# Kernel optimization log

Hardware: AMD Instinct MI355X
Metric: run time of the kernel (lower is better)

## Reference

```python
import jax, jax.numpy as jnp
import numpy as np

ANGLE_BITS = 3          # TurboQuantConfig.angle_bits default
LEVELS = 2 ** ANGLE_BITS
PI = np.pi


def _angle_ranges(d_minus_1, dtype):
    # hyperspherical coords: first d-2 angles in [0, pi], last angle in [0, 2*pi)
    return jnp.concatenate([
        jnp.full((d_minus_1 - 1,), PI, dtype),
        jnp.full((1,), 2.0 * PI, dtype),
    ])


def polar_compress(x):
    """x: [..., d] -> (r [...,1], theta_indices int32 [..., d-1])."""
    # suffix norms s_i = ||x[i:]|| via reversed cumsum of squares
    suffix = jnp.sqrt(jnp.cumsum((x * x)[..., ::-1], axis=-1)[..., ::-1])
    r = suffix[..., :1]
    cos_t = jnp.clip(x[..., :-1] / jnp.maximum(suffix[..., :-1], 1e-12), -1.0, 1.0)
    theta = jnp.arccos(cos_t)                      # [..., d-1], in [0, pi]
    # last angle carries the sign of x[..., -1]: map to [0, 2*pi)
    last = jnp.where(x[..., -1:] < 0, 2.0 * PI - theta[..., -1:], theta[..., -1:])
    theta = jnp.concatenate([theta[..., :-1], last], axis=-1)
    ranges = _angle_ranges(theta.shape[-1], theta.dtype)
    idx = jnp.round(theta / ranges * (LEVELS - 1)).astype(jnp.int32)
    return r, idx


def polar_decompress(r, idx):
    """(r [...,1], idx [..., d-1]) -> x_hat [..., d] via trig products."""
    d1 = idx.shape[-1]
    ranges = _angle_ranges(d1, r.dtype)
    theta = idx.astype(r.dtype) / (LEVELS - 1) * ranges
    sinp = jnp.cumprod(jnp.sin(theta), axis=-1)                 # [..., d-1]
    prods = jnp.concatenate([jnp.ones_like(r), sinp], axis=-1)  # [..., d]
    coss = jnp.concatenate([jnp.cos(theta), jnp.ones_like(r)], axis=-1)
    return r * prods * coss


def setup_inputs() -> dict:
    key = jax.random.key(0)
    kq, kk, kv, kn = jax.random.split(key, 4)
    B, H, T, k, d = 1, 32, 8192, 16, 128
    return {
        "queries": jax.random.normal(kq, (B, H, k, d), jnp.float32),
        "keys": jax.random.normal(kk, (B, H, T, d), jnp.float32),
        "values": jax.random.normal(kv, (B, H, T, d), jnp.float32),
        # faithful stand-in for `torch.randn_like(scores) * 0.01` QJL correction,
        # materialized deterministically as an input
        "qjl_noise": jax.random.normal(kn, (B, H, k, T), jnp.float32) * 0.01,
    }


def reference(queries, keys, values, qjl_noise):
    d = queries.shape[-1]
    # compress_kv_cache: polar angle quantization of keys and values
    r_k, idx_k = polar_compress(keys)
    r_v, idx_v = polar_compress(values)
    # compute_attention_with_compressed_kv: decompress-then-attend
    keys_polar = polar_decompress(r_k, idx_k)      # [B,H,T,d]
    values_polar = polar_decompress(r_v, idx_v)    # [B,H,T,d]
    scores = jnp.einsum('bhkd,bhtd->bhkt', queries, keys_polar) / jnp.sqrt(
        jnp.asarray(d, queries.dtype))
    scores = scores + qjl_noise
    attn = jax.nn.softmax(scores, axis=-1)
    return jnp.einsum('bhkt,bhtd->bhkd', attn, values_polar)
```

## Files before the change

kernel.cpp:

```cpp
#include <hip/hip_runtime.h>
#include <math.h>

typedef __attribute__((ext_vector_type(8))) short bf16x8;
typedef __attribute__((ext_vector_type(4))) float f32x4;
typedef __attribute__((ext_vector_type(2))) float f32x2;

#define HEADS 32
#define SEQT  8192
#define DIM   128
#define NQ    16
#define BPH   64
#define BTOK  128
#define WTOK  32
#define TILE  16
#define NPART BPH
#define PSTR  132
#define QPAD  136
#define QSCALE 0.08838834764831845f

#define OFF_QS    0
#define OFF_PS    4352
#define OFF_LUT   8448
#define OFF_ML    8576
#define OFF_KS    9088
#define OFF_MERGE 9088
#define LDS_BYTES 26496

#define DPP_ROW_SHL(N) (0x100 | (N))
#define DPP_ROW_SHR(N) (0x110 | (N))
#define DPP_QP_XOR1   0xB1
#define DPP_QP_XOR2   0x4E
#define DPP_HALF_MIRR 0x141
#define DPP_MIRR      0x140

template <int CTRL>
__device__ __forceinline__ float dpp0(float v) {
  return __int_as_float(__builtin_amdgcn_update_dpp(
      0, __float_as_int(v), CTRL, 0xF, 0xF, true));
}
template <int CTRL>
__device__ __forceinline__ float dpp1(float v) {
  return __int_as_float(__builtin_amdgcn_update_dpp(
      __float_as_int(1.0f), __float_as_int(v), CTRL, 0xF, 0xF, false));
}
__device__ __forceinline__ float rmax16(float v) {
  v = fmaxf(v, dpp0<DPP_QP_XOR1>(v));
  v = fmaxf(v, dpp0<DPP_QP_XOR2>(v));
  v = fmaxf(v, dpp0<DPP_HALF_MIRR>(v));
  v = fmaxf(v, dpp0<DPP_MIRR>(v));
  return v;
}
__device__ __forceinline__ float rsum16(float v) {
  v += dpp0<DPP_QP_XOR1>(v);
  v += dpp0<DPP_QP_XOR2>(v);
  v += dpp0<DPP_HALF_MIRR>(v);
  v += dpp0<DPP_MIRR>(v);
  return v;
}
__device__ __forceinline__ float rdlane(float v, int l) {
  return __int_as_float(__builtin_amdgcn_readlane(__float_as_int(v), l));
}
__device__ __forceinline__ unsigned short f2bf(float f) {
  unsigned u = __float_as_uint(f);
  u += 0x7FFFu + ((u >> 16) & 1u);
  return (unsigned short)(u >> 16);
}
__device__ __forceinline__ int idx7c(float c) {
  int i = 0;
  i += c <  0.9749279121818236f;
  i += c <  0.7818314824680298f;
  i += c <  0.4338837391175581f;
  i += c <  6.123233995736766e-17f;
  i += c < -0.4338837391175581f;
  i += c < -0.7818314824680298f;
  i += c < -0.9749279121818236f;
  return i;
}

__device__ __forceinline__ float2 polar_rt(float x0, float x1, int lane,
                                           const float2* lutA, const float2* lutB) {
  float a = x0 * x0;
  float p = fmaf(x1, x1, a);
  float v = p;
  v += dpp0<DPP_ROW_SHL(1)>(v);
  v += dpp0<DPP_ROW_SHL(2)>(v);
  v += dpp0<DPP_ROW_SHL(4)>(v);
  v += dpp0<DPP_ROW_SHL(8)>(v);
  float R0 = rdlane(v, 0), R1 = rdlane(v, 16), R2 = rdlane(v, 32), R3 = rdlane(v, 48);
  float T2 = R3, T1 = R2 + R3, T0 = R1 + T1;
  int row = lane >> 4;
  float T = (row == 0) ? T0 : ((row == 1) ? T1 : ((row == 2) ? T2 : 0.f));
  float ss0 = v + T;
  float total = R0 + T0;
  float ss1 = ss0 - a;
  float c0 = x0 * __builtin_amdgcn_rsqf(ss0);
  float c1 = x1 * __builtin_amdgcn_rsqf(ss1);
  float rad = sqrtf(total);
  float2 sc0 = lutA[idx7c(c0)];
  float2 sc1 = lutA[idx7c(c1)];
  if (lane == 63) {
    int ib = 0;
    ib += c0 <  0.9009688679024191f;
    ib += c0 <  0.2225209339563144f;
    ib += c0 < -0.6234898018587336f;
    int i0 = (x1 < 0.f) ? (7 - ib) : ib;
    sc0 = lutB[i0];
    sc1 = make_float2(1.f, 1.f);
  }
  float qp = sc0.x * sc1.x;
  float w = qp;
  w *= dpp1<DPP_ROW_SHR(1)>(w);
  w *= dpp1<DPP_ROW_SHR(2)>(w);
  w *= dpp1<DPP_ROW_SHR(4)>(w);
  w *= dpp1<DPP_ROW_SHR(8)>(w);
  float e = dpp1<DPP_ROW_SHR(1)>(w);
  float F0 = rdlane(w, 15), F1 = rdlane(w, 31), F2 = rdlane(w, 47);
  float M1 = F0, M2 = F0 * F1, M3 = M2 * F2;
  float M = (row == 0) ? 1.f : ((row == 1) ? M1 : ((row == 2) ? M2 : M3));
  float E = e * M;
  float rE = rad * E;
  return make_float2(rE * sc0.y, rE * sc0.x * sc1.y);
}

__global__ __launch_bounds__(256, 4)
void attn_partial(const float* __restrict__ Q, const float* __restrict__ K,
                  const float* __restrict__ V, const float* __restrict__ noise,
                  float* __restrict__ part) {
  __shared__ __align__(16) char RAW[LDS_BYTES];
  unsigned short* Qs  = (unsigned short*)(RAW + OFF_QS);
  float*          Ps  = (float*)(RAW + OFF_PS);
  float2*         lutA = (float2*)(RAW + OFF_LUT);
  float2*         lutB = lutA + 8;
  float2*         Ml  = (float2*)(RAW + OFF_ML);
  unsigned short* Ks  = (unsigned short*)(RAW + OFF_KS);

  const int tid  = threadIdx.x;
  const int lane = tid & 63;
  const int wv   = tid >> 6;
  const int h    = blockIdx.x / BPH;
  const int bh   = blockIdx.x % BPH;

  if (tid < 8) {
    float fi = (float)tid / 7.0f;
    float ta = fi * 3.14159274101257324f;
    float tb = fi * 6.28318548202514648f;
    lutA[tid] = make_float2(sinf(ta), cosf(ta));
    lutB[tid] = make_float2(sinf(tb), cosf(tb));
  }
  {
    const float* Qh = Q + (size_t)h * NQ * DIM;
    for (int i = tid; i < NQ * DIM; i += 256)
      Qs[(i >> 7) * QPAD + (i & 127)] = f2bf(Qh[i] * QSCALE);
  }
  __syncthreads();

  const int G = lane >> 4, r16 = lane & 15;
  bf16x8 qa[4];
#pragma unroll
  for (int c = 0; c < 4; ++c)
    qa[c] = *(const bf16x8*)&Qs[r16 * QPAD + c * 32 + G * 8];

  f32x2 acc[NQ];
#pragma unroll
  for (int qq = 0; qq < NQ; ++qq) acc[qq] = (f32x2){0.f, 0.f};
  float m_r[4] = {-INFINITY, -INFINITY, -INFINITY, -INFINITY};
  float l_r[4] = {0.f, 0.f, 0.f, 0.f};

  const size_t hoff = (size_t)h * SEQT * DIM;
  const int t0 = bh * BTOK + wv * WTOK;
  const float2* Kp = (const float2*)(K + hoff + (size_t)t0 * DIM) + lane;
  const float2* Vp = (const float2*)(V + hoff + (size_t)t0 * DIM) + lane;
  const float* nh = noise + (size_t)h * NQ * SEQT + t0 + r16;
  unsigned short* myK = Ks + wv * TILE * QPAD;
  float* myP = Ps + wv * TILE * NQ;

#pragma unroll 1
  for (int tile = 0; tile < WTOK / TILE; ++tile) {
#pragma unroll 4
    for (int tt = 0; tt < TILE; ++tt) {
      float2 xv = Kp[(tile * TILE + tt) * 64];
      float2 kh = polar_rt(xv.x, xv.y, lane, lutA, lutB);
      unsigned pk = (unsigned)f2bf(kh.x) | ((unsigned)f2bf(kh.y) << 16);
      ((unsigned*)&myK[tt * QPAD])[lane] = pk;
    }
    f32x4 d0 = {0.f, 0.f, 0.f, 0.f};
#pragma unroll
    for (int c = 0; c < 4; ++c) {
      bf16x8 b0 = *(const bf16x8*)&myK[r16 * QPAD + c * 32 + G * 8];
      d0 = __builtin_amdgcn_mfma_f32_16x16x32_bf16(qa[c], b0, d0, 0, 0, 0);
    }
    const float* nt = nh + tile * TILE;
    float s0_[4];
#pragma unroll
    for (int rr = 0; rr < 4; ++rr)
      s0_[rr] = d0[rr] + nt[(size_t)(4 * G + rr) * SEQT];
    float al_r[4];
#pragma unroll
    for (int rr = 0; rr < 4; ++rr) {
      float mt = rmax16(s0_[rr]);
      float mn = fmaxf(m_r[rr], mt);
      al_r[rr] = __expf(m_r[rr] - mn);
      m_r[rr] = mn;
    }
    float p0[4];
#pragma unroll
    for (int rr = 0; rr < 4; ++rr) {
      p0[rr] = __expf(s0_[rr] - m_r[rr]);
      l_r[rr] = l_r[rr] * al_r[rr] + rsum16(p0[rr]);
    }
    *(float4*)&myP[r16 * NQ + 4 * G] = make_float4(p0[0], p0[1], p0[2], p0[3]);
#pragma unroll
    for (int qq = 0; qq < NQ; ++qq) {
      float alq = rdlane(al_r[qq & 3], (qq >> 2) << 4);
      acc[qq] *= (f32x2){alq, alq};
    }
#pragma unroll 2
    for (int tt = 0; tt < TILE; ++tt) {
      float2 xv = Vp[(tile * TILE + tt) * 64];
      float2 vh = polar_rt(xv.x, xv.y, lane, lutA, lutB);
      f32x2 vh2 = {vh.x, vh.y};
      const float* pv = &myP[tt * NQ];
      float4 pa = ((const float4*)pv)[0];
      float4 pb = ((const float4*)pv)[1];
      float4 pc = ((const float4*)pv)[2];
      float4 pd = ((const float4*)pv)[3];
      float pq[NQ] = {pa.x, pa.y, pa.z, pa.w, pb.x, pb.y, pb.z, pb.w,
                      pc.x, pc.y, pc.z, pc.w, pd.x, pd.y, pd.z, pd.w};
#pragma unroll
      for (int qq = 0; qq < NQ; ++qq)
        acc[qq] = __builtin_elementwise_fma((f32x2){pq[qq], pq[qq]}, vh2, acc[qq]);
    }
  }

  if (r16 == 0) {
#pragma unroll
    for (int rr = 0; rr < 4; ++rr)
      Ml[wv * NQ + 4 * G + rr] = make_float2(m_r[rr], l_r[rr]);
  }
  __syncthreads();
#pragma unroll
  for (int qq = 0; qq < NQ; ++qq) {
    float2 e0 = Ml[0 * NQ + qq], e1 = Ml[1 * NQ + qq];
    float2 e2 = Ml[2 * NQ + qq], e3 = Ml[3 * NQ + qq];
    float Mq = fmaxf(fmaxf(e0.x, e1.x), fmaxf(e2.x, e3.x));
    float own = (wv == 0) ? e0.x : ((wv == 1) ? e1.x : ((wv == 2) ? e2.x : e3.x));
    float al = __expf(own - Mq);
    acc[qq] *= (f32x2){al, al};
  }
  float* buf = (float*)(RAW + OFF_MERGE);
  if (wv >= 2) {
#pragma unroll
    for (int qq = 0; qq < NQ; ++qq)
      *(float2*)&buf[(wv - 2) * 2048 + qq * 128 + 2 * lane] =
          make_float2(acc[qq].x, acc[qq].y);
  }
  __syncthreads();
  if (wv < 2) {
#pragma unroll
    for (int qq = 0; qq < NQ; ++qq) {
      float2 t = *(const float2*)&buf[wv * 2048 + qq * 128 + 2 * lane];
      acc[qq] += (f32x2){t.x, t.y};
    }
  }
  __syncthreads();
  if (wv == 1) {
#pragma unroll
    for (int qq = 0; qq < NQ; ++qq)
      *(float2*)&buf[qq * 128 + 2 * lane] = make_float2(acc[qq].x, acc[qq].y);
  }
  __syncthreads();
  if (wv == 0) {
    float* P = part + ((size_t)h * NPART + bh) * (NQ * PSTR);
#pragma unroll
    for (int qq = 0; qq < NQ; ++qq) {
      float2 t = *(const float2*)&buf[qq * 128 + 2 * lane];
      *(float2*)&P[qq * PSTR + 4 + 2 * lane] =
          make_float2(acc[qq].x + t.x, acc[qq].y + t.y);
      float2 e0 = Ml[0 * NQ + qq], e1 = Ml[1 * NQ + qq];
      float2 e2 = Ml[2 * NQ + qq], e3 = Ml[3 * NQ + qq];
      float Mq = fmaxf(fmaxf(e0.x, e1.x), fmaxf(e2.x, e3.x));
      float Lq = e0.y * __expf(e0.x - Mq) + e1.y * __expf(e1.x - Mq) +
                 e2.y * __expf(e2.x - Mq) + e3.y * __expf(e3.x - Mq);
      if (lane == 0) *(float2*)&P[qq * PSTR] = make_float2(Mq, Lq);
    }
  }
}

__global__ __launch_bounds__(128)
void attn_reduce(const float* __restrict__ part, float* __restrict__ out) {
  __shared__ float wgt[NPART];
  __shared__ float Lsh;
  const int tid = threadIdx.x;
  const int h = blockIdx.x >> 4;
  const int q = blockIdx.x & 15;
  const float* P = part + (size_t)h * NPART * NQ * PSTR;
  if (tid < NPART) {
    float2 ml = *(const float2*)&P[((size_t)tid * NQ + q) * PSTR];
    float M = ml.x;
#pragma unroll
    for (int off = 1; off < 64; off <<= 1)
      M = fmaxf(M, __shfl_xor(M, off, 64));
    float w = __expf(ml.x - M);
    wgt[tid] = w;
    float L = ml.y * w;
#pragma unroll
    for (int off = 1; off < 64; off <<= 1)
      L += __shfl_xor(L, off, 64);
    if (tid == 0) Lsh = L;
  }
  __syncthreads();
  const float* A = P + (size_t)q * PSTR + 4 + tid;
  float o = 0.f;
#pragma unroll 8
  for (int c = 0; c < NPART; ++c)
    o = fmaf(wgt[c], A[(size_t)c * NQ * PSTR], o);
  out[((size_t)h * NQ + q) * DIM + tid] = o * (1.0f / Lsh);
}

extern "C" void kernel_launch(void* const* d_in, const int* in_sizes, int n_in,
                              void* d_out, int out_size, void* d_ws, size_t ws_size,
                              hipStream_t stream) {
  (void)in_sizes; (void)n_in; (void)out_size; (void)ws_size;
  const float* Q = (const float*)d_in[0];
  const float* K = (const float*)d_in[1];
  const float* V = (const float*)d_in[2];
  const float* noise = (const float*)d_in[3];
  float* part = (float*)d_ws;
  attn_partial<<<dim3(HEADS * BPH), dim3(256), 0, stream>>>(Q, K, V, noise, part);
  attn_reduce<<<dim3(HEADS * NQ), dim3(128), 0, stream>>>(part, (float*)d_out);
}
```

Measured before the change: 369.6 us.

## Stage K/V via async global-to-LDS loads and decompress 16 dims per lane

Replaces the per-token, whole-wave polar reconstruction (one float2 per lane, cross-lane DPP scans per token) with a layout where each lane handles 16 consecutive dimensions of one token, 8 tokens per pass. Angle bins are found by comparing squared values against squared thresholds, with no LUT. Raw K/V rows are staged into swizzled LDS with global_load_lds, and the next chunk's load is issued during the current decompression to overlap memory with compute. This raises LDS use and lowers launch bounds to 2 blocks per CU, trading occupancy for fewer cross-lane ops and better latency hiding.

```diff
diff --git a/kernel.cpp b/kernel.cpp
--- a/kernel.cpp
+++ b/kernel.cpp
@@ -12,7 +12,7 @@
 #define BPH   64
 #define BTOK  128
 #define WTOK  32
-#define TILE  16
+#define CHK   16
 #define NPART BPH
 #define PSTR  132
 #define QPAD  136
@@ -20,16 +20,32 @@
 
 #define OFF_QS    0
 #define OFF_PS    4352
-#define OFF_LUT   8448
-#define OFF_ML    8576
-#define OFF_KS    9088
-#define OFF_MERGE 9088
-#define LDS_BYTES 26496
-
-#define DPP_ROW_SHL(N) (0x100 | (N))
-#define DPP_ROW_SHR(N) (0x110 | (N))
-#define DPP_QP_XOR1   0xB1
-#define DPP_QP_XOR2   0x4E
+#define OFF_ML    8448
+#define OFF_RAW   8960
+#define OFF_KS    41728
+#define OFF_MERGE 8960
+#define LDS_BYTES 59136
+
+#define W1SQ 0.9504844339512096f
+#define W2SQ 0.6112604669781572f
+#define W3SQ 0.1882550990706332f
+#define S1C  0.4338837391175581f
+#define S2C  0.7818314824680298f
+#define S3C  0.9749279121818236f
+#define C1C  0.9009688679024191f
+#define C2C  0.6234898018587336f
+#define C3C  0.2225209339563144f
+#define B1SQ 0.8117449009293667f
+#define B2SQ 0.0495155660487913f
+#define B3SQ 0.3887395330218429f
+
+#define DPP_QP_XOR1 0xB1
+#define DPP_QP_XOR2 0x4E
+#define DPP_QP_SHL1 0x39
+#define DPP_QP_SHR1 0x90
+#define DPP_QP_SHR2 0x44
+#define DPP_QP_BC0  0x00
+#define DPP_QP_BC3  0xFF
 #define DPP_HALF_MIRR 0x141
 #define DPP_MIRR      0x140
 
@@ -37,11 +53,6 @@
 __device__ __forceinline__ float dpp0(float v) {
   return __int_as_float(__builtin_amdgcn_update_dpp(
       0, __float_as_int(v), CTRL, 0xF, 0xF, true));
-}
-template <int CTRL>
-__device__ __forceinline__ float dpp1(float v) {
-  return __int_as_float(__builtin_amdgcn_update_dpp(
-      __float_as_int(1.0f), __float_as_int(v), CTRL, 0xF, 0xF, false));
 }
 __device__ __forceinline__ float rmax16(float v) {
   v = fmaxf(v, dpp0<DPP_QP_XOR1>(v));
@@ -65,88 +76,165 @@
   u += 0x7FFFu + ((u >> 16) & 1u);
   return (unsigned short)(u >> 16);
 }
-__device__ __forceinline__ int idx7c(float c) {
-  int i = 0;
-  i += c <  0.9749279121818236f;
-  i += c <  0.7818314824680298f;
-  i += c <  0.4338837391175581f;
-  i += c <  6.123233995736766e-17f;
-  i += c < -0.4338837391175581f;
-  i += c < -0.7818314824680298f;
-  i += c < -0.9749279121818236f;
-  return i;
-}
-
-__device__ __forceinline__ float2 polar_rt(float x0, float x1, int lane,
-                                           const float2* lutA, const float2* lutB) {
-  float a = x0 * x0;
-  float p = fmaf(x1, x1, a);
-  float v = p;
-  v += dpp0<DPP_ROW_SHL(1)>(v);
-  v += dpp0<DPP_ROW_SHL(2)>(v);
-  v += dpp0<DPP_ROW_SHL(4)>(v);
-  v += dpp0<DPP_ROW_SHL(8)>(v);
-  float R0 = rdlane(v, 0), R1 = rdlane(v, 16), R2 = rdlane(v, 32), R3 = rdlane(v, 48);
-  float T2 = R3, T1 = R2 + R3, T0 = R1 + T1;
-  int row = lane >> 4;
-  float T = (row == 0) ? T0 : ((row == 1) ? T1 : ((row == 2) ? T2 : 0.f));
-  float ss0 = v + T;
-  float total = R0 + T0;
-  float ss1 = ss0 - a;
-  float c0 = x0 * __builtin_amdgcn_rsqf(ss0);
-  float c1 = x1 * __builtin_amdgcn_rsqf(ss1);
-  float rad = sqrtf(total);
-  float2 sc0 = lutA[idx7c(c0)];
-  float2 sc1 = lutA[idx7c(c1)];
-  if (lane == 63) {
-    int ib = 0;
-    ib += c0 <  0.9009688679024191f;
-    ib += c0 <  0.2225209339563144f;
-    ib += c0 < -0.6234898018587336f;
-    int i0 = (x1 < 0.f) ? (7 - ib) : ib;
-    sc0 = lutB[i0];
-    sc1 = make_float2(1.f, 1.f);
-  }
-  float qp = sc0.x * sc1.x;
-  float w = qp;
-  w *= dpp1<DPP_ROW_SHR(1)>(w);
-  w *= dpp1<DPP_ROW_SHR(2)>(w);
-  w *= dpp1<DPP_ROW_SHR(4)>(w);
-  w *= dpp1<DPP_ROW_SHR(8)>(w);
-  float e = dpp1<DPP_ROW_SHR(1)>(w);
-  float F0 = rdlane(w, 15), F1 = rdlane(w, 31), F2 = rdlane(w, 47);
-  float M1 = F0, M2 = F0 * F1, M3 = M2 * F2;
-  float M = (row == 0) ? 1.f : ((row == 1) ? M1 : ((row == 2) ? M2 : M3));
-  float E = e * M;
-  float rE = rad * E;
-  return make_float2(rE * sc0.y, rE * sc0.x * sc1.y);
-}
-
-__global__ __launch_bounds__(256, 4)
+__device__ __forceinline__ unsigned cvtpk(float lo, float hi) {
+  unsigned r;
+  asm("v_cvt_pk_bf16_f32 %0, %1, %2" : "=v"(r) : "v"(lo), "v"(hi));
+  return r;
+}
+
+__device__ __forceinline__ void stage16(const float* __restrict__ g, char* lds, int lane) {
+  const int h2 = lane >> 5;
+  const int qs = (lane >> 3) & 3;
+  const int js = lane & 7;
+#pragma unroll
+  for (int i = 0; i < 8; ++i) {
+    const int t = 2 * i + h2;
+    const int sb = js ^ (t & 7);
+    __builtin_amdgcn_global_load_lds(
+        (const float*)(g + (size_t)t * DIM + qs * 32 + sb * 4),
+        (float*)(lds + i * 1024), 16, 0, 0);
+  }
+}
+
+template <bool KOUT>
+__device__ __forceinline__ void decomp8(
+    const float* __restrict__ rawW, int sc, int lane,
+    unsigned short* __restrict__ KsW, float* __restrict__ VsW,
+    const float* __restrict__ nextsrc, char* __restrict__ rawBytes)
+{
+  const int tloc = lane >> 3;
+  const int o    = lane & 7;
+  const int T    = sc * 8 + tloc;
+
+  float x[16];
+#pragma unroll
+  for (int j = 0; j < 4; ++j) {
+    const int s = ((o >> 1) << 3) | ((((o & 1) << 2) | j) ^ tloc);
+    const float4 v = *(const float4*)(rawW + T * 128 + 4 * s);
+    x[4*j+0] = v.x; x[4*j+1] = v.y; x[4*j+2] = v.z; x[4*j+3] = v.w;
+  }
+  float qa0 = 0.f, qa1 = 0.f;
+#pragma unroll
+  for (int i = 0; i < 16; i += 2) {
+    qa0 = fmaf(x[i], x[i], qa0);
+    qa1 = fmaf(x[i+1], x[i+1], qa1);
+  }
+  const float qs = qa0 + qa1;
+  const float a1 = dpp0<DPP_QP_SHL1>(qs);
+  const float t1 = qs + (((lane & 3) == 3) ? 0.f : a1);
+  const float b1 = dpp0<DPP_QP_XOR2>(t1);
+  const float t2 = t1 + (((lane & 3) < 2) ? b1 : 0.f);
+  const float qt = dpp0<DPP_QP_BC0>(t2);
+  const float ot = dpp0<DPP_HALF_MIRR>(qt);
+  const float total = qt + ot;
+  const float S = t2 + ((o < 4) ? ot : 0.f);
+
+  if (nextsrc) {
+    __builtin_amdgcn_sched_barrier(0);
+    stage16(nextsrc, nextsrc ? rawBytes : rawBytes, lane);
+  }
+
+  const float r = sqrtf(total);
+
+  float run = S, psin = 1.f, run14 = 0.f;
+  float sv[16], cv[16];
+#pragma unroll
+  for (int i = 0; i < 16; ++i) {
+    const float u = x[i] * x[i];
+    if (i == 14) run14 = run;
+    const bool lo2 = u < W2SQ * run;
+    const float thr = lo2 ? W3SQ : W1SQ;
+    const bool bx = u < thr * run;
+    const float ssin = lo2 ? (bx ? S3C : S2C) : (bx ? S1C : 0.f);
+    float scos = lo2 ? (bx ? C3C : C2C) : (bx ? C1C : 1.f);
+    scos = copysignf(scos, x[i]);
+    sv[i] = ssin; cv[i] = scos;
+    psin *= ssin;
+    run -= u;
+  }
+  const float p1 = dpp0<DPP_QP_SHR1>(psin);
+  const float e1 = psin * (((lane & 3) == 0) ? 1.f : p1);
+  const float p2 = dpp0<DPP_QP_SHR2>(e1);
+  const float e2 = e1 * (((lane & 3) < 2) ? 1.f : p2);
+  const float pq = dpp0<DPP_QP_BC3>(e2);
+  const float po = dpp0<DPP_HALF_MIRR>(pq);
+  const float e3 = e2 * ((o >= 4) ? po : 1.f);
+  const float sh = dpp0<DPP_QP_SHR1>(e3);
+  const float E = ((lane & 3) == 0) ? ((o < 4) ? 1.f : po) : sh;
+
+  float rcum = r * E;
+  unsigned short* krow = KsW + T * QPAD + o * 16;
+  float* vrow = VsW + tloc * 132 + o * 16;
+#pragma unroll
+  for (int g = 0; g < 2; ++g) {
+    float outv[8];
+    float rc14 = rcum;
+#pragma unroll
+    for (int k = 0; k < 8; ++k) {
+      const int i = 8 * g + k;
+      if (i == 14) rc14 = rcum;
+      outv[k] = rcum * cv[i];
+      rcum *= sv[i];
+    }
+    if (g == 1) {
+      const float u14 = x[14] * x[14];
+      const bool neg = x[14] < 0.f;
+      const bool cc1 = u14 < B1SQ * run14;
+      const bool cc2 = u14 < B2SQ * run14;
+      const bool cc3 = u14 > B3SQ * run14;
+      const float cpos = cc2 ? -C3C : (cc1 ? C2C : 1.f);
+      const float spos = cc2 ? S3C : (cc1 ? S2C : 0.f);
+      const float cneg = cc3 ? -C1C : -C3C;
+      const float sneg = cc3 ? S1C : S3C;
+      const float cB = neg ? cneg : cpos;
+      float sB = neg ? sneg : spos;
+      sB = copysignf(sB, x[15]);
+      const bool o7 = (o == 7);
+      outv[6] = o7 ? rc14 * cB : outv[6];
+      outv[7] = o7 ? rc14 * sB : outv[7];
+    }
+    if (KOUT) {
+      uint4 w;
+      w.x = cvtpk(outv[0], outv[1]);
+      w.y = cvtpk(outv[2], outv[3]);
+      w.z = cvtpk(outv[4], outv[5]);
+      w.w = cvtpk(outv[6], outv[7]);
+      *(uint4*)&krow[8 * g] = w;
+    } else {
+      *(float4*)&vrow[8 * g]     = make_float4(outv[0], outv[1], outv[2], outv[3]);
+      *(float4*)&vrow[8 * g + 4] = make_float4(outv[4], outv[5], outv[6], outv[7]);
+    }
+  }
+}
+
+__global__ __launch_bounds__(256, 2)
 void attn_partial(const float* __restrict__ Q, const float* __restrict__ K,
                   const float* __restrict__ V, const float* __restrict__ noise,
                   float* __restrict__ part) {
   __shared__ __align__(16) char RAW[LDS_BYTES];
-  unsigned short* Qs  = (unsigned short*)(RAW + OFF_QS);
-  float*          Ps  = (float*)(RAW + OFF_PS);
-  float2*         lutA = (float2*)(RAW + OFF_LUT);
-  float2*         lutB = lutA + 8;
-  float2*         Ml  = (float2*)(RAW + OFF_ML);
-  unsigned short* Ks  = (unsigned short*)(RAW + OFF_KS);
+  unsigned short* Qs = (unsigned short*)(RAW + OFF_QS);
+  float*          Ps = (float*)(RAW + OFF_PS);
+  float2*         Ml = (float2*)(RAW + OFF_ML);
 
   const int tid  = threadIdx.x;
   const int lane = tid & 63;
   const int wv   = tid >> 6;
   const int h    = blockIdx.x / BPH;
   const int bh   = blockIdx.x % BPH;
-
-  if (tid < 8) {
-    float fi = (float)tid / 7.0f;
-    float ta = fi * 3.14159274101257324f;
-    float tb = fi * 6.28318548202514648f;
-    lutA[tid] = make_float2(sinf(ta), cosf(ta));
-    lutB[tid] = make_float2(sinf(tb), cosf(tb));
-  }
+  const int r16  = lane & 15, G = lane >> 4;
+
+  char* rawB = RAW + OFF_RAW + wv * 8192;
+  const float* rawW = (const float*)rawB;
+  unsigned short* KsW = (unsigned short*)(RAW + OFF_KS + wv * 4352);
+  float* VsW = (float*)KsW;
+  float* myP = Ps + wv * (CHK * NQ);
+
+  const size_t hoff = (size_t)h * SEQT * DIM;
+  const int t0 = bh * BTOK + wv * WTOK;
+  const float* Kg = K + hoff + (size_t)t0 * DIM;
+  const float* Vg = V + hoff + (size_t)t0 * DIM;
+
+  stage16(Kg, rawB, lane);
   {
     const float* Qh = Q + (size_t)h * NQ * DIM;
     for (int i = tid; i < NQ * DIM; i += 256)
@@ -154,7 +242,6 @@
   }
   __syncthreads();
 
-  const int G = lane >> 4, r16 = lane & 15;
   bf16x8 qa[4];
 #pragma unroll
   for (int c = 0; c < 4; ++c)
@@ -166,30 +253,24 @@
   float m_r[4] = {-INFINITY, -INFINITY, -INFINITY, -INFINITY};
   float l_r[4] = {0.f, 0.f, 0.f, 0.f};
 
-  const size_t hoff = (size_t)h * SEQT * DIM;
-  const int t0 = bh * BTOK + wv * WTOK;
-  const float2* Kp = (const float2*)(K + hoff + (size_t)t0 * DIM) + lane;
-  const float2* Vp = (const float2*)(V + hoff + (size_t)t0 * DIM) + lane;
   const float* nh = noise + (size_t)h * NQ * SEQT + t0 + r16;
-  unsigned short* myK = Ks + wv * TILE * QPAD;
-  float* myP = Ps + wv * TILE * NQ;
 
 #pragma unroll 1
-  for (int tile = 0; tile < WTOK / TILE; ++tile) {
-#pragma unroll 4
-    for (int tt = 0; tt < TILE; ++tt) {
-      float2 xv = Kp[(tile * TILE + tt) * 64];
-      float2 kh = polar_rt(xv.x, xv.y, lane, lutA, lutB);
-      unsigned pk = (unsigned)f2bf(kh.x) | ((unsigned)f2bf(kh.y) << 16);
-      ((unsigned*)&myK[tt * QPAD])[lane] = pk;
-    }
+  for (int ch = 0; ch < 2; ++ch) {
+    asm volatile("s_waitcnt vmcnt(0)" ::: "memory");
+
+    const float* Vsrc = Vg + (size_t)ch * CHK * DIM;
+#pragma unroll 1
+    for (int sc = 0; sc < 2; ++sc)
+      decomp8<true>(rawW, sc, lane, KsW, VsW, (sc == 1) ? Vsrc : nullptr, rawB);
+
     f32x4 d0 = {0.f, 0.f, 0.f, 0.f};
 #pragma unroll
     for (int c = 0; c < 4; ++c) {
-      bf16x8 b0 = *(const bf16x8*)&myK[r16 * QPAD + c * 32 + G * 8];
+      bf16x8 b0 = *(const bf16x8*)&KsW[r16 * QPAD + c * 32 + G * 8];
       d0 = __builtin_amdgcn_mfma_f32_16x16x32_bf16(qa[c], b0, d0, 0, 0, 0);
     }
-    const float* nt = nh + tile * TILE;
+    const float* nt = nh + ch * CHK;
     float s0_[4];
 #pragma unroll
     for (int rr = 0; rr < 4; ++rr)
@@ -214,21 +295,28 @@
       float alq = rdlane(al_r[qq & 3], (qq >> 2) << 4);
       acc[qq] *= (f32x2){alq, alq};
     }
+
+    asm volatile("s_waitcnt vmcnt(0)" ::: "memory");
+
+    const float* Knext = (ch == 0) ? (Kg + CHK * DIM) : nullptr;
+#pragma unroll 1
+    for (int sc = 0; sc < 2; ++sc) {
+      decomp8<false>(rawW, sc, lane, KsW, VsW, (sc == 1) ? Knext : nullptr, rawB);
 #pragma unroll 2
-    for (int tt = 0; tt < TILE; ++tt) {
-      float2 xv = Vp[(tile * TILE + tt) * 64];
-      float2 vh = polar_rt(xv.x, xv.y, lane, lutA, lutB);
-      f32x2 vh2 = {vh.x, vh.y};
-      const float* pv = &myP[tt * NQ];
-      float4 pa = ((const float4*)pv)[0];
-      float4 pb = ((const float4*)pv)[1];
-      float4 pc = ((const float4*)pv)[2];
-      float4 pd = ((const float4*)pv)[3];
-      float pq[NQ] = {pa.x, pa.y, pa.z, pa.w, pb.x, pb.y, pb.z, pb.w,
-                      pc.x, pc.y, pc.z, pc.w, pd.x, pd.y, pd.z, pd.w};
-#pragma unroll
-      for (int qq = 0; qq < NQ; ++qq)
-        acc[qq] = __builtin_elementwise_fma((f32x2){pq[qq], pq[qq]}, vh2, acc[qq]);
+      for (int tt = 0; tt < 8; ++tt) {
+        float2 vh = *(const float2*)&VsW[tt * 132 + 2 * lane];
+        f32x2 vh2 = {vh.x, vh.y};
+        const float* pv = &myP[(sc * 8 + tt) * NQ];
+        float4 pa = ((const float4*)pv)[0];
+        float4 pb = ((const float4*)pv)[1];
+        float4 pc = ((const float4*)pv)[2];
+        float4 pd = ((const float4*)pv)[3];
+        float pq[NQ] = {pa.x, pa.y, pa.z, pa.w, pb.x, pb.y, pb.z, pb.w,
+                        pc.x, pc.y, pc.z, pc.w, pd.x, pd.y, pd.z, pd.w};
+#pragma unroll
+        for (int qq = 0; qq < NQ; ++qq)
+          acc[qq] = __builtin_elementwise_fma((f32x2){pq[qq], pq[qq]}, vh2, acc[qq]);
+      }
     }
   }
 
```

Result: faster. 310.3 us (-16.1%).
